# Optimization experiments

Measured on AMD Instinct MI355X. Metric: run time of the kernel, lower is better.

The kernel has to match this reference:

```python
import jax, jax.numpy as jnp
import numpy as np

B, S, D, H = 4, 2048, 1024, 16
DK = D // H


def setup_inputs() -> dict:
    key = jax.random.key(0)
    ks = jax.random.split(key, 5)
    scale = 1.0 / np.sqrt(D)
    return {
        "embeddings": jax.random.normal(ks[0], (B, S, D), dtype=jnp.float32),
        "W_q": jax.random.normal(ks[1], (D, D), dtype=jnp.float32) * scale,
        "W_k": jax.random.normal(ks[2], (D, D), dtype=jnp.float32) * scale,
        "W_v": jax.random.normal(ks[3], (D, D), dtype=jnp.float32) * scale,
        "W_o": jax.random.normal(ks[4], (D, D), dtype=jnp.float32) * scale,
    }


def reference(embeddings, W_q, W_k, W_v, W_o):
    # torch Linear: y = x @ W.T  (weights stored [out, in])
    def proj(x, W):
        # [B,S,D] -> [B,H,S,DK]
        y = jnp.einsum("bsd,ed->bse", x, W)
        return y.reshape(B, S, H, DK).transpose(0, 2, 1, 3)

    Q = proj(embeddings, W_q)
    K = proj(embeddings, W_k)
    V = proj(embeddings, W_v)

    scores = jnp.einsum("bhqd,bhkd->bhqk", Q, K) / jnp.sqrt(jnp.float32(DK))
    p_attn = jax.nn.softmax(scores, axis=-1)  # dropout p=0.0 -> identity
    x = jnp.einsum("bhqk,bhkd->bhqd", p_attn, V)
    x = x.transpose(0, 2, 1, 3).reshape(B, S, D)
    return jnp.einsum("bsd,ed->bse", x, W_o)
```

## Files before the change

kernel.cpp:

```cpp
#include <hip/hip_runtime.h>
#include <hip/hip_bf16.h>

#define BB 4
#define SS 2048
#define DD 1024
#define HH 16
#define MM (BB * SS)

typedef __attribute__((ext_vector_type(8))) short bf16x8;
typedef __attribute__((ext_vector_type(4))) float f32x4;

__device__ __forceinline__ unsigned short f2bf(float f) {
  union { float f; unsigned u; } v; v.f = f;
  unsigned r = v.u + 0x7fffu + ((v.u >> 16) & 1u);
  return (unsigned short)(r >> 16);
}

__device__ __forceinline__ void gl2lds16(const void* g, void* l) {
  __builtin_amdgcn_global_load_lds(
      (const __attribute__((address_space(1))) unsigned int*)g,
      (__attribute__((address_space(3))) unsigned int*)l, 16, 0, 0);
}

__global__ __launch_bounds__(256)
void convall(const float* __restrict__ X, const float* __restrict__ a,
             const float* __restrict__ b, const float* __restrict__ c,
             const float* __restrict__ d, unsigned short* __restrict__ wall,
             unsigned short* __restrict__ xb) {
  int y = blockIdx.y;
  const float* s; unsigned short* o; float scl = 1.0f;
  if (y < 4) {
    const float* srcs[4] = {a, b, c, d};
    s = srcs[y]; o = wall + (size_t)y * 1048576;
    if (y == 0) scl = 0.180336880f;
  } else {
    s = X + (size_t)(y - 4) * 1048576; o = xb + (size_t)(y - 4) * 1048576;
  }
  int i = (blockIdx.x * 256 + threadIdx.x) * 4;
  float4 v = *(const float4*)(s + i);
  ushort4 h4;
  h4.x = f2bf(v.x * scl); h4.y = f2bf(v.y * scl);
  h4.z = f2bf(v.z * scl); h4.w = f2bf(v.w * scl);
  *(ushort4*)(o + i) = h4;
}

template<int OMODE>
__global__ __launch_bounds__(256)
void gemm_k(const unsigned short* __restrict__ A16, const unsigned short* __restrict__ Bp,
            void* __restrict__ C0p, void* __restrict__ C1p, void* __restrict__ C2p) {
  __shared__ unsigned short As[32 * 136];
  __shared__ unsigned short Bs[128 * 32];
  const int m0 = blockIdx.x * 128, n0g = blockIdx.y * 128;
  const int tid = threadIdx.x, lane = tid & 63, wave = tid >> 6;
  const int wm = (wave & 1) * 64, wn = (wave >> 1) * 64;
  const int row_in = lane & 15, quad = lane >> 4;

  f32x4 acc[4][4] = {};

  for (int kb = 0; kb < DD; kb += 32) {
    {
      int r = wave * 32 + (lane >> 2);
      const unsigned short* g = Bp + (size_t)(n0g + r) * DD + kb + (lane & 3) * 8;
      gl2lds16(g, Bs + (wave * 32) * 32);
      gl2lds16(g + (size_t)16 * DD, Bs + (wave * 32 + 16) * 32);
      const unsigned short* ga = A16 + (size_t)(m0 + r) * DD + kb + (lane & 3) * 8;
      gl2lds16(ga, As + (wave * 32) * 32);
      gl2lds16(ga + (size_t)16 * DD, As + (wave * 32 + 16) * 32);
    }
    __syncthreads();
    bf16x8 af[4], bfr[4];
#pragma unroll
    for (int i = 0; i < 4; ++i)
      af[i] = *(const bf16x8*)(As + (wm + i * 16 + row_in) * 32 + quad * 8);
#pragma unroll
    for (int j = 0; j < 4; ++j)
      bfr[j] = *(const bf16x8*)(Bs + (wn + j * 16 + row_in) * 32 + quad * 8);
#pragma unroll
    for (int i = 0; i < 4; ++i)
#pragma unroll
      for (int j = 0; j < 4; ++j)
        acc[i][j] = __builtin_amdgcn_mfma_f32_16x16x32_bf16(af[i], bfr[j], acc[i][j], 0, 0, 0);
    __syncthreads();
  }

  if (OMODE == 1) {
    float* Cout = (float*)C0p;
#pragma unroll
    for (int i = 0; i < 4; ++i)
#pragma unroll
      for (int j = 0; j < 4; ++j)
#pragma unroll
        for (int r = 0; r < 4; ++r)
          Cout[(size_t)(m0 + wm + i * 16 + quad * 4 + r) * DD + n0g + wn + j * 16 + row_in] =
              acc[i][j][r];
  } else {
    const int seg = n0g >> 10;
    if (seg < 2) {
      unsigned short* Cout = (unsigned short*)(seg == 0 ? C0p : C1p);
      const int n0 = n0g & 1023;
#pragma unroll
      for (int i = 0; i < 4; ++i)
#pragma unroll
        for (int j = 0; j < 4; ++j)
#pragma unroll
          for (int r = 0; r < 4; ++r)
            Cout[(size_t)(m0 + wm + i * 16 + quad * 4 + r) * DD + n0 + wn + j * 16 + row_in] =
                f2bf(acc[i][j][r]);
    } else {
      unsigned short* Vt = (unsigned short*)C2p;
      unsigned short* Ts = As;
      const int b = m0 >> 11, m_in_b = m0 & 2047;
      const int nv = n0g - 2048;
#pragma unroll
      for (int cn = 0; cn < 4; ++cn) {
        if ((wave >> 1) == (cn >> 1)) {
#pragma unroll
          for (int i = 0; i < 4; ++i)
#pragma unroll
            for (int jj = 0; jj < 2; ++jj)
#pragma unroll
              for (int r = 0; r < 4; ++r) {
                int j = (cn & 1) * 2 + jj;
                Ts[(jj * 16 + row_in) * 136 + wm + i * 16 + quad * 4 + r] = f2bf(acc[i][j][r]);
              }
        }
        __syncthreads();
#pragma unroll
        for (int it = 0; it < 2; ++it) {
          int cc = tid + it * 256;
          int rowL = cc >> 4, o8 = (cc & 15) * 8;
          int cbase = rowL * 136 + (o8 & 64) + ((o8 & 63) >> 2);
          ushort4 lo, hi;
          lo.x = Ts[cbase];      lo.y = Ts[cbase + 16];
          lo.z = Ts[cbase + 32]; lo.w = Ts[cbase + 48];
          hi.x = Ts[cbase + 1];  hi.y = Ts[cbase + 17];
          hi.z = Ts[cbase + 33]; hi.w = Ts[cbase + 49];
          int n = nv + cn * 32 + rowL;
          int h = n >> 6, dd = n & 63;
          unsigned short* dst = Vt + ((size_t)((b * 16 + h) * 64 + dd)) * SS + m_in_b + o8;
          *(ushort4*)dst = lo;
          *(ushort4*)(dst + 4) = hi;
        }
        __syncthreads();
      }
    }
  }
}

__global__ __launch_bounds__(256, 4)
void attn_kernel(const unsigned short* __restrict__ Q, const unsigned short* __restrict__ K,
                 const unsigned short* __restrict__ Vt_g, unsigned short* __restrict__ AO) {
  __shared__ unsigned short Ks[64 * 72];
  __shared__ unsigned short Vs[64 * 72];
  __shared__ unsigned short Ps[128 * 72];
  const int L = (blockIdx.y << 4) + blockIdx.x;
  const int jj = L >> 3;
  const int qt = jj & 15;
  const int bh = (L & 7) + ((jj >> 4) << 3);
  const int b = bh >> 4, h = bh & 15;
  const int tid = threadIdx.x, lane = tid & 63, w = tid >> 6;
  const int row_in = lane & 15, quad = lane >> 4;
  const size_t qbase = ((size_t)(b * SS + qt * 128)) * DD + h * 64;

  bf16x8 aq[2][2];
#pragma unroll
  for (int m = 0; m < 2; ++m) {
    const unsigned short* qp = Q + qbase + (size_t)(w * 32 + m * 16 + row_in) * DD;
    aq[m][0] = *(const bf16x8*)(qp + quad * 8);
    aq[m][1] = *(const bf16x8*)(qp + 32 + quad * 8);
  }
  f32x4 oacc[2][4] = {};
  float lrow[2][4] = {};
  const int permr = 2 * (row_in >> 2) + (row_in & 1) + 8 * ((row_in >> 1) & 1);
  const int pw_base = (w * 32) * 72;

  const int r0 = tid >> 3, o80 = (tid & 7) * 8;
  const int r1 = (tid + 256) >> 3, o81 = o80;
  const unsigned short* kp0 = K + ((size_t)(b * SS + r0)) * DD + h * 64 + o80;
  const unsigned short* kp1 = K + ((size_t)(b * SS + r1)) * DD + h * 64 + o81;
  const unsigned short* vp0 = Vt_g + ((size_t)(bh * 64 + r0)) * SS + o80;
  const unsigned short* vp1 = Vt_g + ((size_t)(bh * 64 + r1)) * SS + o81;

  uint4 kr0 = *(const uint4*)kp0;
  uint4 kr1 = *(const uint4*)kp1;
  uint4 vr0 = *(const uint4*)vp0;
  uint4 vr1 = *(const uint4*)vp1;

  for (int kt = 0; kt < SS / 64; ++kt) {
    __syncthreads();
    *(uint4*)(Ks + r0 * 72 + o80) = kr0;
    *(uint4*)(Ks + r1 * 72 + o81) = kr1;
    *(uint4*)(Vs + r0 * 72 + o80) = vr0;
    *(uint4*)(Vs + r1 * 72 + o81) = vr1;
    __syncthreads();
    if (kt + 1 < SS / 64) {
      const size_t ko = (size_t)(kt + 1) * 64 * DD;
      const size_t vo = (size_t)(kt + 1) * 64;
      kr0 = *(const uint4*)(kp0 + ko);
      kr1 = *(const uint4*)(kp1 + ko);
      vr0 = *(const uint4*)(vp0 + vo);
      vr1 = *(const uint4*)(vp1 + vo);
    }

    f32x4 sacc[2][4] = {};
    __builtin_amdgcn_s_setprio(1);
#pragma unroll
    for (int n = 0; n < 4; ++n) {
      bf16x8 bk0 = *(const bf16x8*)(Ks + (n * 16 + row_in) * 72 + quad * 8);
      bf16x8 bk1 = *(const bf16x8*)(Ks + (n * 16 + row_in) * 72 + 32 + quad * 8);
#pragma unroll
      for (int m = 0; m < 2; ++m) {
        sacc[m][n] = __builtin_amdgcn_mfma_f32_16x16x32_bf16(aq[m][0], bk0, sacc[m][n], 0, 0, 0);
        sacc[m][n] = __builtin_amdgcn_mfma_f32_16x16x32_bf16(aq[m][1], bk1, sacc[m][n], 0, 0, 0);
      }
    }
    __builtin_amdgcn_s_setprio(0);

#pragma unroll
    for (int m = 0; m < 2; ++m)
#pragma unroll
      for (int r = 0; r < 4; ++r) {
        int prow = pw_base + (m * 16 + 2 * quad + (r & 1) + 8 * ((r >> 1) & 1)) * 72;
        union { float f; unsigned u; } p0, p1, p2, p3;
        p0.f = __builtin_amdgcn_exp2f(sacc[m][0][r]);
        p1.f = __builtin_amdgcn_exp2f(sacc[m][1][r]);
        p2.f = __builtin_amdgcn_exp2f(sacc[m][2][r]);
        p3.f = __builtin_amdgcn_exp2f(sacc[m][3][r]);
        lrow[m][r] += (p0.f + p1.f) + (p2.f + p3.f);
        unsigned w01 = __builtin_amdgcn_perm(p1.u + 0x8000u, p0.u + 0x8000u, 0x07060302);
        unsigned w23 = __builtin_amdgcn_perm(p3.u + 0x8000u, p2.u + 0x8000u, 0x07060302);
        *(uint2*)(Ps + prow + row_in * 4) = make_uint2(w01, w23);
      }

    __builtin_amdgcn_s_setprio(1);
#pragma unroll
    for (int c = 0; c < 2; ++c) {
      bf16x8 ap0 = *(const bf16x8*)(Ps + pw_base + (permr) * 72 + c * 32 + quad * 8);
      bf16x8 ap1 = *(const bf16x8*)(Ps + pw_base + (16 + permr) * 72 + c * 32 + quad * 8);
#pragma unroll
      for (int t = 0; t < 4; ++t) {
        bf16x8 bv = *(const bf16x8*)(Vs + (t * 16 + row_in) * 72 + c * 32 + quad * 8);
        oacc[0][t] = __builtin_amdgcn_mfma_f32_16x16x32_bf16(ap0, bv, oacc[0][t], 0, 0, 0);
        oacc[1][t] = __builtin_amdgcn_mfma_f32_16x16x32_bf16(ap1, bv, oacc[1][t], 0, 0, 0);
      }
    }
    __builtin_amdgcn_s_setprio(0);
  }

#pragma unroll
  for (int m = 0; m < 2; ++m)
#pragma unroll
    for (int r = 0; r < 4; ++r) {
#pragma unroll
      for (int s = 1; s < 16; s <<= 1) lrow[m][r] += __shfl_xor(lrow[m][r], s, 64);
      float inv = 1.0f / lrow[m][r];
#pragma unroll
      for (int t = 0; t < 4; ++t)
        AO[qbase + (size_t)(w * 32 + m * 16 + quad * 4 + r) * DD + t * 16 + row_in] =
            f2bf(oacc[m][t][r] * inv);
    }
}

extern "C" void kernel_launch(void* const* d_in, const int* in_sizes, int n_in,
                              void* d_out, int out_size, void* d_ws, size_t ws_size,
                              hipStream_t stream) {
  const float* X  = (const float*)d_in[0];
  const float* Wq = (const float*)d_in[1];
  const float* Wk = (const float*)d_in[2];
  const float* Wv = (const float*)d_in[3];
  const float* Wo = (const float*)d_in[4];

  unsigned short* ws   = (unsigned short*)d_ws;
  unsigned short* Qb   = ws;
  unsigned short* Kb   = Qb + (size_t)MM * DD;
  unsigned short* Vtb  = Kb + (size_t)MM * DD;
  unsigned short* Wall = Vtb + (size_t)MM * DD;
  unsigned short* Xb   = (unsigned short*)d_out;
  float* out = (float*)d_out;

  convall<<<dim3(1024, 12), 256, 0, stream>>>(X, Wq, Wk, Wv, Wo, Wall, Xb);

  gemm_k<3><<<dim3(MM / 128, 24), 256, 0, stream>>>(Xb, Wall, Qb, Kb, Vtb);

  attn_kernel<<<dim3(SS / 128, BB * HH), 256, 0, stream>>>(Qb, Kb, Vtb, Qb);

  gemm_k<1><<<dim3(MM / 128, 8), 256, 0, stream>>>(Qb, Wall + (size_t)3 * 1048576,
                                                   out, nullptr, nullptr);
}
```

Measured before the change: 267.9 us.

## Double-buffer LDS tiles in projection GEMM and raise priority around MFMA

Converts the GEMM main loop to ping-pong LDS buffers, issuing the next K-tile's global-to-LDS loads before computing on the current tile and dropping one barrier per iteration. It also sets wave priority high during the MFMA block. This aims to hide global load latency behind matrix math, at the cost of doubled LDS usage and reliance on barrier waitcnt semantics for correctness.

```diff
diff --git a/kernel.cpp b/kernel.cpp
--- a/kernel.cpp
+++ b/kernel.cpp
@@ -48,8 +48,8 @@
 __global__ __launch_bounds__(256)
 void gemm_k(const unsigned short* __restrict__ A16, const unsigned short* __restrict__ Bp,
             void* __restrict__ C0p, void* __restrict__ C1p, void* __restrict__ C2p) {
-  __shared__ unsigned short As[32 * 136];
-  __shared__ unsigned short Bs[128 * 32];
+  __shared__ unsigned short As[2 * 4096];
+  __shared__ unsigned short Bs[2 * 4096];
   const int m0 = blockIdx.x * 128, n0g = blockIdx.y * 128;
   const int tid = threadIdx.x, lane = tid & 63, wave = tid >> 6;
   const int wm = (wave & 1) * 64, wn = (wave >> 1) * 64;
@@ -57,31 +57,43 @@
 
   f32x4 acc[4][4] = {};
 
+  const int r = wave * 32 + (lane >> 2);
+  const unsigned short* gB = Bp + (size_t)(n0g + r) * DD + (lane & 3) * 8;
+  const unsigned short* gA = A16 + (size_t)(m0 + r) * DD + (lane & 3) * 8;
+
+  gl2lds16(gB, Bs + (wave * 32) * 32);
+  gl2lds16(gB + (size_t)16 * DD, Bs + (wave * 32 + 16) * 32);
+  gl2lds16(gA, As + (wave * 32) * 32);
+  gl2lds16(gA + (size_t)16 * DD, As + (wave * 32 + 16) * 32);
+
+  int cur = 0;
   for (int kb = 0; kb < DD; kb += 32) {
-    {
-      int r = wave * 32 + (lane >> 2);
-      const unsigned short* g = Bp + (size_t)(n0g + r) * DD + kb + (lane & 3) * 8;
-      gl2lds16(g, Bs + (wave * 32) * 32);
-      gl2lds16(g + (size_t)16 * DD, Bs + (wave * 32 + 16) * 32);
-      const unsigned short* ga = A16 + (size_t)(m0 + r) * DD + kb + (lane & 3) * 8;
-      gl2lds16(ga, As + (wave * 32) * 32);
-      gl2lds16(ga + (size_t)16 * DD, As + (wave * 32 + 16) * 32);
-    }
     __syncthreads();
+    if (kb + 32 < DD) {
+      const int nx = (cur ^ 1) * 4096;
+      gl2lds16(gB + kb + 32, Bs + nx + (wave * 32) * 32);
+      gl2lds16(gB + kb + 32 + (size_t)16 * DD, Bs + nx + (wave * 32 + 16) * 32);
+      gl2lds16(gA + kb + 32, As + nx + (wave * 32) * 32);
+      gl2lds16(gA + kb + 32 + (size_t)16 * DD, As + nx + (wave * 32 + 16) * 32);
+    }
+    const int cb = cur * 4096;
     bf16x8 af[4], bfr[4];
 #pragma unroll
     for (int i = 0; i < 4; ++i)
-      af[i] = *(const bf16x8*)(As + (wm + i * 16 + row_in) * 32 + quad * 8);
+      af[i] = *(const bf16x8*)(As + cb + (wm + i * 16 + row_in) * 32 + quad * 8);
 #pragma unroll
     for (int j = 0; j < 4; ++j)
-      bfr[j] = *(const bf16x8*)(Bs + (wn + j * 16 + row_in) * 32 + quad * 8);
+      bfr[j] = *(const bf16x8*)(Bs + cb + (wn + j * 16 + row_in) * 32 + quad * 8);
+    __builtin_amdgcn_s_setprio(1);
 #pragma unroll
     for (int i = 0; i < 4; ++i)
 #pragma unroll
       for (int j = 0; j < 4; ++j)
         acc[i][j] = __builtin_amdgcn_mfma_f32_16x16x32_bf16(af[i], bfr[j], acc[i][j], 0, 0, 0);
-    __syncthreads();
-  }
+    __builtin_amdgcn_s_setprio(0);
+    cur ^= 1;
+  }
+  __syncthreads();
 
   if (OMODE == 1) {
     float* Cout = (float*)C0p;
@@ -90,9 +102,9 @@
 #pragma unroll
       for (int j = 0; j < 4; ++j)
 #pragma unroll
-        for (int r = 0; r < 4; ++r)
-          Cout[(size_t)(m0 + wm + i * 16 + quad * 4 + r) * DD + n0g + wn + j * 16 + row_in] =
-              acc[i][j][r];
+        for (int r2 = 0; r2 < 4; ++r2)
+          Cout[(size_t)(m0 + wm + i * 16 + quad * 4 + r2) * DD + n0g + wn + j * 16 + row_in] =
+              acc[i][j][r2];
   } else {
     const int seg = n0g >> 10;
     if (seg < 2) {
@@ -103,9 +115,9 @@
 #pragma unroll
         for (int j = 0; j < 4; ++j)
 #pragma unroll
-          for (int r = 0; r < 4; ++r)
-            Cout[(size_t)(m0 + wm + i * 16 + quad * 4 + r) * DD + n0 + wn + j * 16 + row_in] =
-                f2bf(acc[i][j][r]);
+          for (int r2 = 0; r2 < 4; ++r2)
+            Cout[(size_t)(m0 + wm + i * 16 + quad * 4 + r2) * DD + n0 + wn + j * 16 + row_in] =
+                f2bf(acc[i][j][r2]);
     } else {
       unsigned short* Vt = (unsigned short*)C2p;
       unsigned short* Ts = As;
@@ -119,9 +131,9 @@
 #pragma unroll
             for (int jj = 0; jj < 2; ++jj)
 #pragma unroll
-              for (int r = 0; r < 4; ++r) {
+              for (int r2 = 0; r2 < 4; ++r2) {
                 int j = (cn & 1) * 2 + jj;
-                Ts[(jj * 16 + row_in) * 136 + wm + i * 16 + quad * 4 + r] = f2bf(acc[i][j][r]);
+                Ts[(jj * 16 + row_in) * 136 + wm + i * 16 + quad * 4 + r2] = f2bf(acc[i][j][r2]);
               }
         }
         __syncthreads();
```

After: 263.2 us. Within noise of the previous version (-1.8%).
